# Performance work log

Measured on AMD Instinct MI355X. Metric: run time of the kernel, lower is better.

The kernel has to match this reference:

```python
import jax, jax.numpy as jnp
import numpy as np

NPOINT, RADIUS, NSAMPLE = 1024, 0.2, 32


def _fps(xyz, npoint):
    # xyz: (B, N, 3) -> (B, npoint) int32, iterative furthest point sampling
    B, N, _ = xyz.shape

    def step(carry, _):
        dists, far = carry  # (B,N), (B,)
        centroid = jnp.take_along_axis(xyz, far[:, None, None], axis=1)  # (B,1,3)
        d = jnp.sum((xyz - centroid) ** 2, axis=-1)  # (B,N)
        dists = jnp.minimum(dists, d)
        nxt = jnp.argmax(dists, axis=-1).astype(jnp.int32)
        return (dists, nxt), far

    init = (jnp.full((B, N), 1e10, xyz.dtype), jnp.zeros((B,), jnp.int32))
    _, idx = jax.lax.scan(step, init, None, length=npoint)
    return jnp.transpose(idx)  # (B, npoint)


def _ball_query(radius, nsample, xyz, new_xyz):
    # xyz: (B,N,3), new_xyz: (B,S,3) -> (B,S,nsample) int32
    N = xyz.shape[1]
    d2 = jnp.sum((new_xyz[:, :, None, :] - xyz[:, None, :, :]) ** 2, axis=-1)  # (B,S,N)
    # first-nsample-in-range semantics of PointNet++ ball_query
    key = jnp.where(d2 < radius * radius, jnp.arange(N, dtype=jnp.int32), N)
    neg, order = jax.lax.top_k(-key, nsample)  # smallest keys first
    valid = (-neg) < N
    return jnp.where(valid, order, order[..., :1])  # pad with first valid idx


def _group(feat, idx):
    # feat: (B,D,N), idx: (B,S,ns) -> (B,D,S,ns)
    return jax.vmap(lambda f, i: f[:, i])(feat, idx)


def _conv(x, w, b):
    # 1x1 Conv2d: x (B,C,S,ns), w (O,C), b (O)
    return jnp.einsum('oc,bcps->bops', w, x) + b[None, :, None, None]


def _bn(x, s, t):
    # inference BatchNorm folded into per-channel affine
    return x * s[None, :, None, None] + t[None, :, None, None]


def setup_inputs() -> dict:
    key = jax.random.key(0)
    ks = jax.random.split(key, 40)
    B, N, D = 16, 8192, 64
    BCH = 8  # max(8, 64 // 8)

    def w(k, shape, scale=0.1):
        return jax.random.normal(k, shape, jnp.float32) * scale

    def bn(k, c):
        k1, k2 = jax.random.split(k)
        return (jax.random.uniform(k1, (c,), jnp.float32, 0.75, 1.25),
                0.1 * jax.random.normal(k2, (c,), jnp.float32))

    attn_s0, attn_t0 = bn(ks[2], BCH)
    attn_s1, attn_t1 = bn(ks[3], D)
    attn_s2, attn_t2 = bn(ks[4], D)
    mlp_s0, mlp_t0 = bn(ks[5], 64)
    mlp_s1, mlp_t1 = bn(ks[6], 64)
    eca_s, eca_t = bn(ks[7], 128)
    return {
        'xyz': jax.random.uniform(ks[0], (B, 3, N), jnp.float32),
        'points': jax.random.normal(ks[1], (B, D, N), jnp.float32),
        'attn_w0': w(ks[10], (BCH, 3)), 'attn_b0': w(ks[11], (BCH,)),
        'attn_s0': attn_s0, 'attn_t0': attn_t0,
        'attn_w1': w(ks[12], (D, BCH)), 'attn_b1': w(ks[13], (D,)),
        'attn_s1': attn_s1, 'attn_t1': attn_t1,
        'attn_w2': w(ks[14], (D, D)), 'attn_b2': w(ks[15], (D,)),
        'attn_s2': attn_s2, 'attn_t2': attn_t2,
        'mlp_w0': w(ks[16], (64, D)), 'mlp_b0': w(ks[17], (64,)),
        'mlp_s0': mlp_s0, 'mlp_t0': mlp_t0,
        'mlp_w1': w(ks[18], (64, 64)), 'mlp_b1': w(ks[19], (64,)),
        'mlp_s1': mlp_s1, 'mlp_t1': mlp_t1,
        'eca_k': w(ks[20], (3,), 0.5),
        'eca_w': w(ks[21], (128, 64)), 'eca_b': w(ks[22], (128,)),
        'eca_s': eca_s, 'eca_t': eca_t,
    }


def reference(xyz, points,
              attn_w0, attn_b0, attn_s0, attn_t0,
              attn_w1, attn_b1, attn_s1, attn_t1,
              attn_w2, attn_b2, attn_s2, attn_t2,
              mlp_w0, mlp_b0, mlp_s0, mlp_t0,
              mlp_w1, mlp_b1, mlp_s1, mlp_t1,
              eca_k, eca_w, eca_b, eca_s, eca_t):
    xyz_f = jnp.transpose(xyz, (0, 2, 1))  # (B,N,3)
    # 1. sampling + grouping
    fps_idx = _fps(xyz_f, NPOINT)  # (B,S)
    new_xyz = jax.vmap(lambda p, i: p[:, i])(xyz, fps_idx)  # (B,3,S)
    idx = _ball_query(RADIUS, NSAMPLE, xyz_f, jnp.transpose(new_xyz, (0, 2, 1)))
    grouped_xyz = _group(xyz, idx) - new_xyz[..., None]  # (B,3,S,ns)
    x = _group(points, idx)  # (B,D,S,ns)
    # 2. position-attention module
    pos = jax.nn.relu(_bn(_conv(grouped_xyz, attn_w0, attn_b0), attn_s0, attn_t0))
    pos = _bn(_conv(pos, attn_w1, attn_b1), attn_s1, attn_t1)
    x = x + pos
    x = _bn(_conv(x, attn_w2, attn_b2), attn_s2, attn_t2)
    # 3. shared MLP (conv-bn-relu over mlp[:-1])
    x = jax.nn.relu(_bn(_conv(x, mlp_w0, mlp_b0), mlp_s0, mlp_t0))
    x = jax.nn.relu(_bn(_conv(x, mlp_w1, mlp_b1), mlp_s1, mlp_t1))
    # 4. ECA channel attention + final 1x1 conv-bn
    y = jnp.mean(x, axis=(2, 3))  # (B,C)
    yp = jnp.pad(y, ((0, 0), (1, 1)))
    y = eca_k[0] * yp[:, :-2] + eca_k[1] * yp[:, 1:-1] + eca_k[2] * yp[:, 2:]
    x = x * jax.nn.sigmoid(y)[:, :, None, None]
    x = _bn(_conv(x, eca_w, eca_b), eca_s, eca_t)
    # 5. max-pool over neighborhood
    new_features = jnp.max(x, axis=-1)  # (B,128,S)
    return (new_xyz, new_features)
```

## Files before the change

### kernel.cpp

```cpp
#include <hip/hip_runtime.h>

typedef unsigned int   u32;
typedef unsigned long long u64;
typedef float pkf2 __attribute__((ext_vector_type(2)));

#define B_  16
#define N_  8192
#define S_  1024
#define NS_ 32
#define XS_ 68

__device__ __forceinline__ float nanguard(float v) {
  u32 x = __float_as_uint(v);
  if ((x & 0x7F80u) == 0x7F80u) x ^= 0x0080u;
  return __uint_as_float(x);
}

__device__ __forceinline__ float wave_max_nonneg(float v) {
  int x = __float_as_int(v);
#define DPP_STEP(ctrl) \
  x = __float_as_int(fmaxf(__int_as_float(x), \
      __int_as_float(__builtin_amdgcn_update_dpp(0, x, (ctrl), 0xf, 0xf, true))))
  DPP_STEP(0x111);
  DPP_STEP(0x112);
  DPP_STEP(0x114);
  DPP_STEP(0x118);
  DPP_STEP(0x142);
  DPP_STEP(0x143);
#undef DPP_STEP
  return __int_as_float(__builtin_amdgcn_readlane(x, 63));
}

__global__ __launch_bounds__(256) void k_xyzt(const float* __restrict__ xyz, float4* __restrict__ xyzt) {
  int b = blockIdx.y;
  int i = blockIdx.x * 256 + threadIdx.x;
  const float* p = xyz + (size_t)b * 3 * N_;
  xyzt[(size_t)b * N_ + i] = make_float4(p[i], p[N_ + i], p[2 * N_ + i], 0.f);
}

__global__ __launch_bounds__(256) void k_ptst(const float* __restrict__ pts, float* __restrict__ ptst) {
  __shared__ float tile[64][65];
  int b = blockIdx.y, n0 = blockIdx.x * 64, t = threadIdx.x;
  {
    int c = t >> 2, j0 = (t & 3) * 16;
    const float4* src = (const float4*)(pts + (size_t)b * 64 * N_ + (size_t)c * N_ + n0 + j0);
#pragma unroll
    for (int q = 0; q < 4; ++q) {
      float4 a = src[q];
      tile[c][j0 + 4*q + 0] = a.x; tile[c][j0 + 4*q + 1] = a.y;
      tile[c][j0 + 4*q + 2] = a.z; tile[c][j0 + 4*q + 3] = a.w;
    }
  }
  __syncthreads();
  {
    int n = t >> 2, c0 = (t & 3) * 16;
    float4* dv = (float4*)(ptst + ((size_t)b * N_ + n0 + n) * 64 + c0);
#pragma unroll
    for (int q = 0; q < 4; ++q)
      dv[q] = make_float4(tile[c0 + 4*q + 0][n], tile[c0 + 4*q + 1][n],
                          tile[c0 + 4*q + 2][n], tile[c0 + 4*q + 3][n]);
  }
}

__global__ __launch_bounds__(1024)
__attribute__((amdgpu_waves_per_eu(4, 4)))
void k_fps(const float4* __restrict__ xyzt,
           float4* __restrict__ nxf,
           float* __restrict__ out_xyz) {
#pragma clang fp contract(off)
  __shared__ float4 ldsp[N_];
  __shared__ u64 slot[4];
  __shared__ int win_hist[S_];
  int b = blockIdx.x, t = threadIdx.x;
  const float4* p4 = xyzt + (size_t)b * N_;
  const float4* pp8 = p4 + t * 8;

  float4 q0 = pp8[0], q1 = pp8[1], q2 = pp8[2], q3 = pp8[3];
  float4 q4 = pp8[4], q5 = pp8[5], q6 = pp8[6], q7 = pp8[7];
  ldsp[t * 8 + 0] = q0; ldsp[t * 8 + 1] = q1; ldsp[t * 8 + 2] = q2; ldsp[t * 8 + 3] = q3;
  ldsp[t * 8 + 4] = q4; ldsp[t * 8 + 5] = q5; ldsp[t * 8 + 6] = q6; ldsp[t * 8 + 7] = q7;

#define DECLPAIR(P, A, B) \
  pkf2 px##P = {q##A.x, q##B.x}; pkf2 py##P = {q##A.y, q##B.y}; \
  pkf2 pz##P = {q##A.z, q##B.z}; pkf2 dm##P = {1e10f, 1e10f};
  DECLPAIR(01, 0, 1) DECLPAIR(23, 2, 3) DECLPAIR(45, 4, 5) DECLPAIR(67, 6, 7)
#undef DECLPAIR
#define PIN(P) asm volatile("" : "+v"(px##P), "+v"(py##P), "+v"(pz##P));
  PIN(01) PIN(23) PIN(45) PIN(67)
#undef PIN

  if (t == 0) {
    slot[0] = 8191ull;
    slot[1] = 0; slot[2] = 0; slot[3] = 0;
    win_hist[0] = 0;
  }
  __syncthreads();
  int lane = t & 63;
  for (int it = 1; it < S_; ++it) {
    u64 w = slot[(it - 1) & 3];
    int widx = 8191 - (int)(w & 0xFFFFFFFFull);
    if (t == 0) { win_hist[it - 1] = widx; slot[(it + 1) & 3] = 0; }
    float4 c = ldsp[widx & (N_ - 1)];
    pkf2 cx2 = {c.x, c.x}, cy2 = {c.y, c.y}, cz2 = {c.z, c.z};
#define UPDP(P) { \
    pkf2 dx = px##P - cx2; pkf2 dy = py##P - cy2; pkf2 dz = pz##P - cz2; \
    pkf2 xx = dx * dx; pkf2 yy = dy * dy; pkf2 zz = dz * dz; \
    pkf2 ss = xx + yy; pkf2 dd = ss + zz; \
    dm##P.x = fminf(dm##P.x, dd.x); dm##P.y = fminf(dm##P.y, dd.y); }
    UPDP(01) UPDP(23) UPDP(45) UPDP(67)
#undef UPDP
    float e0 = dm01.x, e1 = dm01.y, e2 = dm23.x, e3 = dm23.y;
    float e4 = dm45.x, e5 = dm45.y, e6 = dm67.x, e7 = dm67.y;
    float va0 = e1 > e0 ? e1 : e0; int ia0 = e1 > e0 ? 1 : 0;
    float va1 = e3 > e2 ? e3 : e2; int ia1 = e3 > e2 ? 3 : 2;
    float va2 = e5 > e4 ? e5 : e4; int ia2 = e5 > e4 ? 5 : 4;
    float va3 = e7 > e6 ? e7 : e6; int ia3 = e7 > e6 ? 7 : 6;
    float vb0 = va1 > va0 ? va1 : va0; int ib0 = va1 > va0 ? ia1 : ia0;
    float vb1 = va3 > va2 ? va3 : va2; int ib1 = va3 > va2 ? ia3 : ia2;
    float bv = vb1 > vb0 ? vb1 : vb0;  int bk = vb1 > vb0 ? ib1 : ib0;
    int bi = t * 8 + bk;
    float wm = wave_max_nonneg(bv);
    u64 msk = __ballot(bv == wm);
    int wl = __ffsll((long long)msk) - 1;
    int wbi = __builtin_amdgcn_readlane(bi, wl);
    if (lane == 0)
      atomicMax(&slot[it & 3],
                ((u64)__float_as_uint(wm) << 32) | (u64)(u32)(8191 - wbi));
    __syncthreads();
  }
  if (t == 0)
    win_hist[S_ - 1] = 8191 - (int)(slot[(S_ - 1) & 3] & 0xFFFFFFFFull);
  __syncthreads();
  {
    int wi = win_hist[t] & (N_ - 1);
    float4 c = ldsp[wi];
    nxf[(size_t)b * S_ + t] = c;
    float* o = out_xyz + (size_t)b * 3 * S_;
    o[t] = nanguard(c.x); o[S_ + t] = nanguard(c.y); o[2 * S_ + t] = nanguard(c.z);
  }
}

__global__ __launch_bounds__(256) void k_ball(const float4* __restrict__ xyzt,
                                              const float4* __restrict__ nxf,
                                              int* __restrict__ ballidx) {
  int gw = blockIdx.x * 4 + (threadIdx.x >> 6);
  int lane = threadIdx.x & 63;
  int b = gw >> 10, s = gw & 1023;
  float4 c = nxf[(size_t)b * S_ + s];
  const float4* pts = xyzt + (size_t)b * N_;
  int* out = ballidx + (size_t)gw * NS_;
  int cnt = 0, first = 0;
  bool havefirst = false;
  for (int chunk = 0; chunk < N_; chunk += 64) {
    float4 p = pts[chunk + lane];
    float dx = p.x - c.x, dy = p.y - c.y, dz = p.z - c.z;
    float d2 = __fadd_rn(__fadd_rn(__fmul_rn(dx, dx), __fmul_rn(dy, dy)), __fmul_rn(dz, dz));
    bool v = d2 <= 0.04f;
    u64 m = __ballot(v);
    if (m) {
      int pos = cnt + __popcll(m & ((1ull << lane) - 1ull));
      if (v && pos < NS_) out[pos] = chunk + lane;
      if (!havefirst) { first = chunk + (__ffsll((long long)m) - 1); havefirst = true; }
      cnt += __popcll(m);
      if (cnt >= NS_) break;
    }
  }
  if (cnt < NS_) {
    for (int p = cnt + lane; p < NS_; p += 64) out[p] = first;
  }
}

struct ChainSm {
  float Wbuf[64 * XS_];
  float W1f[64 * 9];
  float W0f[8 * 4];
  float s2f[64], sm0f[64], sm1f[64];
  float bb0[8];
  float bb1[64], bb2[64], bm0[64], bm1[64];
  float X[32 * XS_];
  float H[32 * XS_];
  float scratch[384];
  int   idx_s[NS_];
};

__device__ __forceinline__ void stage_w64(float* Wbuf, const float* w, int t) {
  int c = t >> 2, q = (t & 3) * 16;
  const float4* src = (const float4*)(w + c * 64 + q);
  float4* dst = (float4*)(Wbuf + c * XS_ + q);
  dst[0] = src[0]; dst[1] = src[1]; dst[2] = src[2]; dst[3] = src[3];
}

template<bool RELU>
__device__ __forceinline__ void gemm64(const float* __restrict__ Wbuf,
                                       const float* __restrict__ Xin,
                                       float* __restrict__ Yout,
                                       const float* __restrict__ scl,
                                       const float* __restrict__ bia,
                                       int lane, int n0) {
  float acc[8] = {0,0,0,0,0,0,0,0};
#pragma unroll
  for (int k4 = 0; k4 < 16; ++k4) {
    float4 wq = *(const float4*)&Wbuf[lane * XS_ + k4 * 4];
#pragma unroll
    for (int nj = 0; nj < 8; ++nj) {
      float4 xq = *(const float4*)&Xin[(n0 + nj) * XS_ + k4 * 4];
      acc[nj] += wq.x * xq.x; acc[nj] += wq.y * xq.y;
      acc[nj] += wq.z * xq.z; acc[nj] += wq.w * xq.w;
    }
  }
  float sc = scl[lane], bi = bia[lane];
#pragma unroll
  for (int nj = 0; nj < 8; ++nj) {
    float v = sc * acc[nj] + bi;
    Yout[(n0 + nj) * XS_ + lane] = RELU ? fmaxf(v, 0.f) : v;
  }
}

template<bool USE_PTST>
__device__ __forceinline__ void chain_tile(ChainSm& sm, int b, int s, int bs,
    const float4* xyzt, const float* ptst, const float* points,
    const float4* nxf, const int* ballidx,
    const float* w0, const float* b0, const float* s0, const float* t0,
    const float* w1, const float* b1, const float* s1, const float* t1,
    const float* w2, const float* b2, const float* s2, const float* t2,
    const float* m0w, const float* m0b, const float* m0s, const float* m0t,
    const float* m1w, const float* m1b, const float* m1s, const float* m1t) {
  int t = threadIdx.x, lane = t & 63, g = t >> 6, n0 = g * 8;

  stage_w64(sm.Wbuf, w2, t);
  if (t < 64) {
    float v2 = s2[t];  sm.s2f[t] = v2;  sm.bb2[t] = v2 * b2[t] + t2[t];
    float vm0 = m0s[t]; sm.sm0f[t] = vm0; sm.bm0[t] = vm0 * m0b[t] + m0t[t];
    float vm1 = m1s[t]; sm.sm1f[t] = vm1; sm.bm1[t] = vm1 * m1b[t] + m1t[t];
    float v1 = s1[t];
#pragma unroll
    for (int k = 0; k < 8; ++k) sm.W1f[t * 9 + k] = v1 * w1[t * 8 + k];
    sm.bb1[t] = v1 * b1[t] + t1[t];
  }
  if (t < 8) {
    float v0 = s0[t];
#pragma unroll
    for (int k = 0; k < 3; ++k) sm.W0f[t * 4 + k] = v0 * w0[t * 3 + k];
    sm.bb0[t] = v0 * b0[t] + t0[t];
  }
  if (t < NS_) sm.idx_s[t] = ballidx[(size_t)bs * NS_ + t] & (N_ - 1);
  __syncthreads();

  {
    int n = t >> 3, c8 = (t & 7) * 8;
    int pi = sm.idx_s[n];
    if (USE_PTST) {
      const float4* v = (const float4*)(ptst + ((size_t)b * N_ + pi) * 64 + c8);
      float4* xr = (float4*)&sm.X[n * XS_ + c8];
      xr[0] = v[0]; xr[1] = v[1];
    } else {
      const float* pp = points + (size_t)b * 64 * N_ + (size_t)c8 * N_ + pi;
#pragma unroll
      for (int j = 0; j < 8; ++j) sm.X[n * XS_ + c8 + j] = pp[(size_t)j * N_];
    }
  }
  if (t < NS_) {
    float4 p = xyzt[(size_t)b * N_ + sm.idx_s[t]];
    float4 cc = nxf[(size_t)b * S_ + s];
    float* gx = &sm.scratch[256 + t * 4];
    gx[0] = p.x - cc.x; gx[1] = p.y - cc.y; gx[2] = p.z - cc.z;
  }
  __syncthreads();

  {
    int n = t >> 3, cc = t & 7;
    const float* gx = &sm.scratch[256 + n * 4];
    float a = sm.bb0[cc];
    a += sm.W0f[cc * 4 + 0] * gx[0];
    a += sm.W0f[cc * 4 + 1] * gx[1];
    a += sm.W0f[cc * 4 + 2] * gx[2];
    sm.scratch[n * 8 + cc] = fmaxf(a, 0.f);
  }
  {
#pragma unroll
    for (int nj = 0; nj < 8; ++nj) {
      float a = sm.bb1[lane];
      const float* p8 = &sm.scratch[(n0 + nj) * 8];
#pragma unroll
      for (int k = 0; k < 8; ++k) a += sm.W1f[lane * 9 + k] * p8[k];
      sm.X[(n0 + nj) * XS_ + lane] += a;
    }
  }
  gemm64<false>(sm.Wbuf, sm.X, sm.H, sm.s2f, sm.bb2, lane, n0);
  __syncthreads();
  stage_w64(sm.Wbuf, m0w, t);
  __syncthreads();
  gemm64<true>(sm.Wbuf, sm.H, sm.X, sm.sm0f, sm.bm0, lane, n0);
  __syncthreads();
  stage_w64(sm.Wbuf, m1w, t);
  __syncthreads();
  gemm64<true>(sm.Wbuf, sm.X, sm.H, sm.sm1f, sm.bm1, lane, n0);
}

template<bool USE_PTST, bool WRITE_H2>
__global__ __launch_bounds__(256) void k_chain(
    const float4* __restrict__ xyzt, const float* __restrict__ ptst,
    const float* __restrict__ points,
    const float4* __restrict__ nxf, const int* __restrict__ ballidx,
    const float* w0, const float* b0, const float* s0, const float* t0,
    const float* w1, const float* b1, const float* s1, const float* t1,
    const float* w2, const float* b2, const float* s2, const float* t2,
    const float* m0w, const float* m0b, const float* m0s, const float* m0t,
    const float* m1w, const float* m1b, const float* m1s, const float* m1t,
    float* __restrict__ h2out, float* __restrict__ partials) {
  __shared__ ChainSm sm;
  int t = threadIdx.x, bs = blockIdx.x;
  int b = bs >> 10, s = bs & 1023;
  int lane = t & 63, g = t >> 6, n0 = g * 8;

  chain_tile<USE_PTST>(sm, b, s, bs, xyzt, ptst, points, nxf, ballidx,
                       w0, b0, s0, t0, w1, b1, s1, t1, w2, b2, s2, t2,
                       m0w, m0b, m0s, m0t, m1w, m1b, m1s, m1t);

  float* psum = sm.scratch;
  float lsum = 0.f;
#pragma unroll
  for (int nj = 0; nj < 8; ++nj) {
    float r = sm.H[(n0 + nj) * XS_ + lane];
    lsum += r;
    if (WRITE_H2)
      h2out[((size_t)bs * 32 + n0 + nj) * 64 + lane] = r;
  }
  psum[lane * 5 + g] = lsum;
  __syncthreads();
  if (t < 64) {
    float v = (psum[t * 5 + 0] + psum[t * 5 + 1]) + (psum[t * 5 + 2] + psum[t * 5 + 3]);
    partials[(size_t)bs * 64 + t] = v;
  }
}

__global__ __launch_bounds__(256) void k_eca(const float* __restrict__ partials,
                                             const float* __restrict__ ecak,
                                             float* __restrict__ sig) {
  __shared__ float red[64 * 5];
  __shared__ float yy[66];
  int b = blockIdx.x, t = threadIdx.x;
  int c = t & 63, sg = t >> 6;
  float acc = 0.f;
  for (int s = sg; s < S_; s += 4) acc += partials[((size_t)b * S_ + s) * 64 + c];
  red[c * 5 + sg] = acc;
  __syncthreads();
  if (t < 64) {
    float v = (red[t * 5 + 0] + red[t * 5 + 1]) + (red[t * 5 + 2] + red[t * 5 + 3]);
    yy[t + 1] = v * (1.f / 32768.f);
  }
  if (t == 64) { yy[0] = 0.f; yy[65] = 0.f; }
  __syncthreads();
  if (t < 64) {
    float gv = ecak[0] * yy[t] + ecak[1] * yy[t + 1] + ecak[2] * yy[t + 2];
    sig[b * 64 + t] = 1.f / (1.f + expf(-gv));
  }
}

__device__ __forceinline__ void final_gemm(const float* __restrict__ WA,
                                           const float* __restrict__ WB,
                                           const float* __restrict__ X2,
                                           const float* __restrict__ esf,
                                           const float* __restrict__ bbf,
                                           float* __restrict__ zred,
                                           float* __restrict__ outf,
                                           int b, int s, int t) {
  int lane = t & 63, g = t >> 6, n0 = g * 8;
  float aA[8] = {0,0,0,0,0,0,0,0}, aB[8] = {0,0,0,0,0,0,0,0};
#pragma unroll
  for (int k4 = 0; k4 < 16; ++k4) {
    float4 wqA = *(const float4*)&WA[lane * XS_ + k4 * 4];
    float4 wqB = *(const float4*)&WB[lane * XS_ + k4 * 4];
#pragma unroll
    for (int nj = 0; nj < 8; ++nj) {
      float4 xq = *(const float4*)&X2[(n0 + nj) * XS_ + k4 * 4];
      aA[nj] += wqA.x * xq.x; aA[nj] += wqA.y * xq.y;
      aA[nj] += wqA.z * xq.z; aA[nj] += wqA.w * xq.w;
      aB[nj] += wqB.x * xq.x; aB[nj] += wqB.y * xq.y;
      aB[nj] += wqB.z * xq.z; aB[nj] += wqB.w * xq.w;
    }
  }
  float mA = aA[0], mB = aB[0];
#pragma unroll
  for (int j = 1; j < 8; ++j) { mA = fmaxf(mA, aA[j]); mB = fmaxf(mB, aB[j]); }
  zred[lane * 5 + g]        = esf[lane] * mA + bbf[lane];
  zred[(lane + 64) * 5 + g] = esf[lane + 64] * mB + bbf[lane + 64];
  __syncthreads();
  if (t < 128) {
    float m = fmaxf(fmaxf(zred[t * 5 + 0], zred[t * 5 + 1]),
                    fmaxf(zred[t * 5 + 2], zred[t * 5 + 3]));
    outf[((size_t)b * 128 + t) * S_ + s] = nanguard(m);
  }
}

__global__ __launch_bounds__(256) void k_final_h2(const float* __restrict__ h2,
                                                  const float* __restrict__ sig,
                                                  const float* ew, const float* eb,
                                                  const float* es, const float* et,
                                                  float* __restrict__ outf) {
  __shared__ float Wh[128 * XS_];
  __shared__ float esf[128], bbf[128], sigl[64];
  __shared__ float X2[32 * XS_];
  __shared__ float zred[128 * 5];
  int t = threadIdx.x, bs = blockIdx.x;
  int b = bs >> 10, s = bs & 1023;
  {
    int c2 = t >> 1, h = (t & 1) * 32;
    const float4* src = (const float4*)(ew + c2 * 64 + h);
    float4* dst = (float4*)(Wh + c2 * XS_ + h);
#pragma unroll
    for (int j = 0; j < 8; ++j) dst[j] = src[j];
  }
  if (t < 128) {
    float v = es[t]; esf[t] = v; bbf[t] = v * eb[t] + et[t];
  }
  if (t < 64) sigl[t] = sig[b * 64 + t];
  __syncthreads();
  {
    int n = t >> 3, c8 = (t & 7) * 8;
    const float4* v = (const float4*)(h2 + ((size_t)bs * 32 + n) * 64 + c8);
    float4 a = v[0], bq = v[1];
    a.x *= sigl[c8 + 0]; a.y *= sigl[c8 + 1]; a.z *= sigl[c8 + 2]; a.w *= sigl[c8 + 3];
    bq.x *= sigl[c8 + 4]; bq.y *= sigl[c8 + 5]; bq.z *= sigl[c8 + 6]; bq.w *= sigl[c8 + 7];
    float4* xr = (float4*)&X2[n * XS_ + c8];
    xr[0] = a; xr[1] = bq;
  }
  final_gemm(Wh, Wh + 64 * XS_, X2, esf, bbf, zred, outf, b, s, t);
}

template<bool USE_PTST>
__global__ __launch_bounds__(256) void k_final_rec(
    const float4* __restrict__ xyzt, const float* __restrict__ ptst,
    const float* __restrict__ points,
    const float4* __restrict__ nxf, const int* __restrict__ ballidx,
    const float* w0, const float* b0, const float* s0, const float* t0,
    const float* w1, const float* b1, const float* s1, const float* t1,
    const float* w2, const float* b2, const float* s2, const float* t2,
    const float* m0w, const float* m0b, const float* m0s, const float* m0t,
    const float* m1w, const float* m1b, const float* m1s, const float* m1t,
    const float* __restrict__ sig,
    const float* ew, const float* eb, const float* es, const float* et,
    float* __restrict__ outf) {
  __shared__ ChainSm sm;
  __shared__ float Wb2[64 * XS_];
  __shared__ float esf2[128], bbf2[128], sigl2[64];
  __shared__ float zred[128 * 5];
  int t = threadIdx.x, bs = blockIdx.x;
  int b = bs >> 10, s = bs & 1023;
  int lane = t & 63, g = t >> 6, n0 = g * 8;

  chain_tile<USE_PTST>(sm, b, s, bs, xyzt, ptst, points, nxf, ballidx,
                       w0, b0, s0, t0, w1, b1, s1, t1, w2, b2, s2, t2,
                       m0w, m0b, m0s, m0t, m1w, m1b, m1s, m1t);

  __syncthreads();
  stage_w64(sm.Wbuf, ew, t);
  stage_w64(Wb2, ew + 64 * 64, t);
  if (t < 128) {
    float v = es[t]; esf2[t] = v; bbf2[t] = v * eb[t] + et[t];
  }
  if (t < 64) sigl2[t] = sig[b * 64 + t];
  __syncthreads();
  {
#pragma unroll
    for (int nj = 0; nj < 8; ++nj)
      sm.X[(n0 + nj) * XS_ + lane] = sigl2[lane] * sm.H[(n0 + nj) * XS_ + lane];
  }
  final_gemm(sm.Wbuf, Wb2, sm.X, esf2, bbf2, zred, outf, b, s, t);
}

extern "C" void kernel_launch(void* const* d_in, const int* in_sizes, int n_in,
                              void* d_out, int out_size, void* d_ws, size_t ws_size,
                              hipStream_t stream) {
  const float* xyz    = (const float*)d_in[0];
  const float* points = (const float*)d_in[1];
  const float* w0 = (const float*)d_in[2],  *b0 = (const float*)d_in[3],  *s0 = (const float*)d_in[4],  *t0 = (const float*)d_in[5];
  const float* w1 = (const float*)d_in[6],  *b1 = (const float*)d_in[7],  *s1 = (const float*)d_in[8],  *t1 = (const float*)d_in[9];
  const float* w2 = (const float*)d_in[10], *b2 = (const float*)d_in[11], *s2 = (const float*)d_in[12], *t2 = (const float*)d_in[13];
  const float* m0w = (const float*)d_in[14], *m0b = (const float*)d_in[15], *m0s = (const float*)d_in[16], *m0t = (const float*)d_in[17];
  const float* m1w = (const float*)d_in[18], *m1b = (const float*)d_in[19], *m1s = (const float*)d_in[20], *m1t = (const float*)d_in[21];
  const float* ecak = (const float*)d_in[22];
  const float* ew = (const float*)d_in[23], *eb = (const float*)d_in[24], *es = (const float*)d_in[25], *et = (const float*)d_in[26];

  const size_t OFF_XYZT = 0;
  const size_t OFF_NXF  = 2097152;
  const size_t OFF_BIDX = 2359296;
  const size_t OFF_PART = 4456448;
  const size_t OFF_SIG  = 8650752;
  const size_t OFF_PTST = 8654848;
  const size_t OFF_H2   = 42209280;
  const size_t NEED_PTST = OFF_H2;
  const size_t NEED_H2   = 176427008;

  const bool use_ptst = ws_size >= NEED_PTST;
  const bool use_h2   = ws_size >= NEED_H2;

  char* ws = (char*)d_ws;
  float4* xyzt    = (float4*)(ws + OFF_XYZT);
  float4* nxf     = (float4*)(ws + OFF_NXF);
  int*    ballidx = (int*)   (ws + OFF_BIDX);
  float*  partials= (float*) (ws + OFF_PART);
  float*  sig     = (float*) (ws + OFF_SIG);
  float*  ptst    = (float*) (ws + OFF_PTST);
  float*  h2      = (float*) (ws + OFF_H2);

  float* out_xyz  = (float*)d_out;
  float* out_feat = (float*)d_out + (size_t)B_ * 3 * S_;

  k_xyzt<<<dim3(N_ / 256, B_), 256, 0, stream>>>(xyz, xyzt);
  if (use_ptst)
    k_ptst<<<dim3(N_ / 64, B_), 256, 0, stream>>>(points, ptst);
  k_fps <<<B_, 1024, 0, stream>>>(xyzt, nxf, out_xyz);
  k_ball<<<(B_ * S_) / 4, 256, 0, stream>>>(xyzt, nxf, ballidx);

  if (use_h2) {
    k_chain<true, true><<<B_ * S_, 256, 0, stream>>>(xyzt, ptst, points, nxf, ballidx,
        w0, b0, s0, t0, w1, b1, s1, t1, w2, b2, s2, t2,
        m0w, m0b, m0s, m0t, m1w, m1b, m1s, m1t, h2, partials);
    k_eca<<<B_, 256, 0, stream>>>(partials, ecak, sig);
    k_final_h2<<<B_ * S_, 256, 0, stream>>>(h2, sig, ew, eb, es, et, out_feat);
  } else if (use_ptst) {
    k_chain<true, false><<<B_ * S_, 256, 0, stream>>>(xyzt, ptst, points, nxf, ballidx,
        w0, b0, s0, t0, w1, b1, s1, t1, w2, b2, s2, t2,
        m0w, m0b, m0s, m0t, m1w, m1b, m1s, m1t, h2, partials);
    k_eca<<<B_, 256, 0, stream>>>(partials, ecak, sig);
    k_final_rec<true><<<B_ * S_, 256, 0, stream>>>(xyzt, ptst, points, nxf, ballidx,
        w0, b0, s0, t0, w1, b1, s1, t1, w2, b2, s2, t2,
        m0w, m0b, m0s, m0t, m1w, m1b, m1s, m1t, sig, ew, eb, es, et, out_feat);
  } else {
    k_chain<false, false><<<B_ * S_, 256, 0, stream>>>(xyzt, ptst, points, nxf, ballidx,
        w0, b0, s0, t0, w1, b1, s1, t1, w2, b2, s2, t2,
        m0w, m0b, m0s, m0t, m1w, m1b, m1s, m1t, h2, partials);
    k_eca<<<B_, 256, 0, stream>>>(partials, ecak, sig);
    k_final_rec<false><<<B_ * S_, 256, 0, stream>>>(xyzt, ptst, points, nxf, ballidx,
        w0, b0, s0, t0, w1, b1, s1, t1, w2, b2, s2, t2,
        m0w, m0b, m0s, m0t, m1w, m1b, m1s, m1t, sig, ew, eb, es, et, out_feat);
  }
}
```

Measured before the change: 1.535 ms.

## Fuse FPS, ball query and MLP chain into one persistent producer-consumer kernel

Replaces the separate FPS, ball-query and chain launches with one persistent kernel. Sixteen blocks run furthest point sampling and publish their progress through global atomic counters. The remaining 240 worker blocks spin-wait on those counters, then run the ball query and the conv/MLP chain for each ready centroid. This overlaps the serial FPS with the per-centroid MLP work, which previously ran strictly after it. In exchange it relies on all blocks being co-resident (deadlock risk if they are not), adds spin-wait overhead, and runs the work blocks at 1024 threads with large LDS use.

```diff
diff --git a/kernel.cpp b/kernel.cpp
--- a/kernel.cpp
+++ b/kernel.cpp
@@ -9,6 +9,8 @@
 #define S_  1024
 #define NS_ 32
 #define XS_ 68
+#define NWORK_ 240
+#define NCHUNK_ 4096
 
 __device__ __forceinline__ float nanguard(float v) {
   u32 x = __float_as_uint(v);
@@ -31,7 +33,9 @@
   return __int_as_float(__builtin_amdgcn_readlane(x, 63));
 }
 
-__global__ __launch_bounds__(256) void k_xyzt(const float* __restrict__ xyz, float4* __restrict__ xyzt) {
+__global__ __launch_bounds__(256) void k_xyzt(const float* __restrict__ xyz, float4* __restrict__ xyzt,
+                                              u32* __restrict__ prog) {
+  if (blockIdx.x == 0 && blockIdx.y == 0 && threadIdx.x < 16) prog[threadIdx.x] = 0u;
   int b = blockIdx.y;
   int i = blockIdx.x * 256 + threadIdx.x;
   const float* p = xyz + (size_t)b * 3 * N_;
@@ -334,6 +338,250 @@
   }
 }
 
+struct ChainSub {
+  float X[32 * XS_];
+  float H[32 * XS_];
+  float scratch[384];
+  int   idx_s[NS_];
+};
+struct WkSm {
+  float Wc2[64 * XS_];
+  float Wm0[64 * XS_];
+  float Wm1[64 * XS_];
+  float W1f[64 * 9];
+  float W0f[8 * 4];
+  float s2f[64], sm0f[64], sm1f[64];
+  float bb0[8];
+  float bb1[64], bb2[64], bm0[64], bm1[64];
+  ChainSub sub[4];
+};
+struct FpsSm {
+  float4 ldsp[N_];
+  u64 slot[4];
+  int win_hist[S_];
+};
+union FusedSm { FpsSm f; WkSm w; };
+static_assert(sizeof(FusedSm) <= 160 * 1024, "LDS overflow");
+
+__global__ __launch_bounds__(1024)
+__attribute__((amdgpu_waves_per_eu(4, 4)))
+void k_fused(const float4* __restrict__ xyzt, const float* __restrict__ ptst,
+             float4* __restrict__ nxf, float* __restrict__ out_xyz,
+             u32* __restrict__ prog,
+             const float* w0, const float* b0, const float* s0, const float* t0,
+             const float* w1, const float* b1, const float* s1, const float* t1,
+             const float* w2, const float* b2, const float* s2, const float* t2,
+             const float* m0w, const float* m0b, const float* m0s, const float* m0t,
+             const float* m1w, const float* m1b, const float* m1s, const float* m1t,
+             float* __restrict__ h2out, float* __restrict__ partials) {
+  __shared__ FusedSm smu;
+  int t = threadIdx.x;
+
+  if (blockIdx.x < B_) {
+#pragma clang fp contract(off)
+    FpsSm& fs = smu.f;
+    int b = blockIdx.x;
+    const float4* p4 = xyzt + (size_t)b * N_;
+    const float4* pp8 = p4 + t * 8;
+
+    float4 q0 = pp8[0], q1 = pp8[1], q2 = pp8[2], q3 = pp8[3];
+    float4 q4 = pp8[4], q5 = pp8[5], q6 = pp8[6], q7 = pp8[7];
+    fs.ldsp[t * 8 + 0] = q0; fs.ldsp[t * 8 + 1] = q1; fs.ldsp[t * 8 + 2] = q2; fs.ldsp[t * 8 + 3] = q3;
+    fs.ldsp[t * 8 + 4] = q4; fs.ldsp[t * 8 + 5] = q5; fs.ldsp[t * 8 + 6] = q6; fs.ldsp[t * 8 + 7] = q7;
+
+#define DECLPAIR(P, A, B) \
+    pkf2 px##P = {q##A.x, q##B.x}; pkf2 py##P = {q##A.y, q##B.y}; \
+    pkf2 pz##P = {q##A.z, q##B.z}; pkf2 dm##P = {1e10f, 1e10f};
+    DECLPAIR(01, 0, 1) DECLPAIR(23, 2, 3) DECLPAIR(45, 4, 5) DECLPAIR(67, 6, 7)
+#undef DECLPAIR
+#define PIN(P) asm volatile("" : "+v"(px##P), "+v"(py##P), "+v"(pz##P));
+    PIN(01) PIN(23) PIN(45) PIN(67)
+#undef PIN
+
+    if (t == 0) {
+      fs.slot[0] = 8191ull;
+      fs.slot[1] = 0; fs.slot[2] = 0; fs.slot[3] = 0;
+      fs.win_hist[0] = 0;
+    }
+    __syncthreads();
+    int lane = t & 63;
+    for (int it = 1; it < S_; ++it) {
+      u64 w = fs.slot[(it - 1) & 3];
+      int widx = 8191 - (int)(w & 0xFFFFFFFFull);
+      float4 c = fs.ldsp[widx & (N_ - 1)];
+      if (t == 0) {
+        fs.win_hist[it - 1] = widx; fs.slot[(it + 1) & 3] = 0;
+        if ((it & 15) == 0)
+          __hip_atomic_store(&prog[b], (u32)(it - 1), __ATOMIC_RELEASE, __HIP_MEMORY_SCOPE_AGENT);
+        nxf[(size_t)b * S_ + (it - 1)] = c;
+      }
+      pkf2 cx2 = {c.x, c.x}, cy2 = {c.y, c.y}, cz2 = {c.z, c.z};
+#define UPDP(P) { \
+      pkf2 dx = px##P - cx2; pkf2 dy = py##P - cy2; pkf2 dz = pz##P - cz2; \
+      pkf2 xx = dx * dx; pkf2 yy = dy * dy; pkf2 zz = dz * dz; \
+      pkf2 ss = xx + yy; pkf2 dd = ss + zz; \
+      dm##P.x = fminf(dm##P.x, dd.x); dm##P.y = fminf(dm##P.y, dd.y); }
+      UPDP(01) UPDP(23) UPDP(45) UPDP(67)
+#undef UPDP
+      float e0 = dm01.x, e1 = dm01.y, e2 = dm23.x, e3 = dm23.y;
+      float e4 = dm45.x, e5 = dm45.y, e6 = dm67.x, e7 = dm67.y;
+      float va0 = e1 > e0 ? e1 : e0; int ia0 = e1 > e0 ? 1 : 0;
+      float va1 = e3 > e2 ? e3 : e2; int ia1 = e3 > e2 ? 3 : 2;
+      float va2 = e5 > e4 ? e5 : e4; int ia2 = e5 > e4 ? 5 : 4;
+      float va3 = e7 > e6 ? e7 : e6; int ia3 = e7 > e6 ? 7 : 6;
+      float vb0 = va1 > va0 ? va1 : va0; int ib0 = va1 > va0 ? ia1 : ia0;
+      float vb1 = va3 > va2 ? va3 : va2; int ib1 = va3 > va2 ? ia3 : ia2;
+      float bv = vb1 > vb0 ? vb1 : vb0;  int bk = vb1 > vb0 ? ib1 : ib0;
+      int bi = t * 8 + bk;
+      float wm = wave_max_nonneg(bv);
+      u64 msk = __ballot(bv == wm);
+      int wl = __ffsll((long long)msk) - 1;
+      int wbi = __builtin_amdgcn_readlane(bi, wl);
+      if (lane == 0)
+        atomicMax(&fs.slot[it & 3],
+                  ((u64)__float_as_uint(wm) << 32) | (u64)(u32)(8191 - wbi));
+      __syncthreads();
+    }
+    if (t == 0) {
+      int wl_ = 8191 - (int)(fs.slot[(S_ - 1) & 3] & 0xFFFFFFFFull);
+      fs.win_hist[S_ - 1] = wl_;
+      float4 c = fs.ldsp[wl_ & (N_ - 1)];
+      nxf[(size_t)b * S_ + (S_ - 1)] = c;
+    }
+    __syncthreads();
+    {
+      int wi = fs.win_hist[t] & (N_ - 1);
+      float4 c = fs.ldsp[wi];
+      float* o = out_xyz + (size_t)b * 3 * S_;
+      o[t] = nanguard(c.x); o[S_ + t] = nanguard(c.y); o[2 * S_ + t] = nanguard(c.z);
+    }
+    if (t == 0)
+      __hip_atomic_store(&prog[b], (u32)S_, __ATOMIC_RELEASE, __HIP_MEMORY_SCOPE_AGENT);
+    return;
+  }
+
+  WkSm& wk = smu.w;
+  int w = blockIdx.x - B_;
+  if (t < 256) {
+    stage_w64(wk.Wc2, w2, t);
+    stage_w64(wk.Wm0, m0w, t);
+    stage_w64(wk.Wm1, m1w, t);
+  }
+  if (t < 64) {
+    float v2 = s2[t];  wk.s2f[t] = v2;  wk.bb2[t] = v2 * b2[t] + t2[t];
+    float vm0 = m0s[t]; wk.sm0f[t] = vm0; wk.bm0[t] = vm0 * m0b[t] + m0t[t];
+    float vm1 = m1s[t]; wk.sm1f[t] = vm1; wk.bm1[t] = vm1 * m1b[t] + m1t[t];
+    float v1 = s1[t];
+#pragma unroll
+    for (int k = 0; k < 8; ++k) wk.W1f[t * 9 + k] = v1 * w1[t * 8 + k];
+    wk.bb1[t] = v1 * b1[t] + t1[t];
+  }
+  if (t < 8) {
+    float v0 = s0[t];
+#pragma unroll
+    for (int k = 0; k < 3; ++k) wk.W0f[t * 4 + k] = v0 * w0[t * 3 + k];
+    wk.bb0[t] = v0 * b0[t] + t0[t];
+  }
+  __syncthreads();
+
+  int sg = t >> 8, tid = t & 255, lane = t & 63, g2 = (t >> 6) & 3, n0 = g2 * 8;
+  ChainSub& cs = wk.sub[sg];
+
+  for (int c = w; c < NCHUNK_; c += NWORK_) {
+    int s = c >> 2, bg = c & 3, b = bg * 4 + sg;
+    if (t == 0) {
+      int bbase = bg * 4;
+#pragma unroll
+      for (int j = 0; j < 4; ++j) {
+        while (__hip_atomic_load(&prog[bbase + j], __ATOMIC_RELAXED, __HIP_MEMORY_SCOPE_AGENT) < (u32)(s + 1))
+          __builtin_amdgcn_s_sleep(32);
+      }
+      (void)__hip_atomic_load(&prog[bbase], __ATOMIC_ACQUIRE, __HIP_MEMORY_SCOPE_AGENT);
+    }
+    __syncthreads();
+
+    float4 cc;
+    if (g2 == 0) {
+      cc = nxf[(size_t)b * S_ + s];
+      const float4* pts = xyzt + (size_t)b * N_;
+      int cnt = 0, first = 0;
+      bool havefirst = false;
+      for (int chunk = 0; chunk < N_; chunk += 64) {
+        float4 p = pts[chunk + lane];
+        float dx = p.x - cc.x, dy = p.y - cc.y, dz = p.z - cc.z;
+        float d2 = __fadd_rn(__fadd_rn(__fmul_rn(dx, dx), __fmul_rn(dy, dy)), __fmul_rn(dz, dz));
+        bool v = d2 <= 0.04f;
+        u64 m = __ballot(v);
+        if (m) {
+          int pos = cnt + __popcll(m & ((1ull << lane) - 1ull));
+          if (v && pos < NS_) cs.idx_s[pos] = chunk + lane;
+          if (!havefirst) { first = chunk + (__ffsll((long long)m) - 1); havefirst = true; }
+          cnt += __popcll(m);
+          if (cnt >= NS_) break;
+        }
+      }
+      if (cnt < NS_) {
+        for (int p = cnt + lane; p < NS_; p += 64) cs.idx_s[p] = first;
+      }
+    }
+    __syncthreads();
+
+    {
+      int n = tid >> 3, c8 = (tid & 7) * 8;
+      int pi = cs.idx_s[n];
+      const float4* v = (const float4*)(ptst + ((size_t)b * N_ + pi) * 64 + c8);
+      float4* xr = (float4*)&cs.X[n * XS_ + c8];
+      xr[0] = v[0]; xr[1] = v[1];
+    }
+    if (tid < NS_) {
+      float4 p = xyzt[(size_t)b * N_ + cs.idx_s[tid]];
+      float* gx = &cs.scratch[256 + tid * 4];
+      gx[0] = p.x - cc.x; gx[1] = p.y - cc.y; gx[2] = p.z - cc.z;
+    }
+    __syncthreads();
+
+    {
+      int n = tid >> 3, ch = tid & 7;
+      const float* gx = &cs.scratch[256 + n * 4];
+      float a = wk.bb0[ch];
+      a += wk.W0f[ch * 4 + 0] * gx[0];
+      a += wk.W0f[ch * 4 + 1] * gx[1];
+      a += wk.W0f[ch * 4 + 2] * gx[2];
+      cs.scratch[n * 8 + ch] = fmaxf(a, 0.f);
+    }
+    {
+#pragma unroll
+      for (int nj = 0; nj < 8; ++nj) {
+        float a = wk.bb1[lane];
+        const float* p8 = &cs.scratch[(n0 + nj) * 8];
+#pragma unroll
+        for (int k = 0; k < 8; ++k) a += wk.W1f[lane * 9 + k] * p8[k];
+        cs.X[(n0 + nj) * XS_ + lane] += a;
+      }
+    }
+    gemm64<false>(wk.Wc2, cs.X, cs.H, wk.s2f, wk.bb2, lane, n0);
+    gemm64<true >(wk.Wm0, cs.H, cs.X, wk.sm0f, wk.bm0, lane, n0);
+    gemm64<true >(wk.Wm1, cs.X, cs.H, wk.sm1f, wk.bm1, lane, n0);
+
+    int bs = (b << 10) | s;
+    float lsum = 0.f;
+#pragma unroll
+    for (int nj = 0; nj < 8; ++nj) {
+      float r = cs.H[(n0 + nj) * XS_ + lane];
+      lsum += r;
+      h2out[((size_t)bs * 32 + n0 + nj) * 64 + lane] = r;
+    }
+    __syncthreads();
+    cs.scratch[lane * 5 + g2] = lsum;
+    __syncthreads();
+    if (tid < 64) {
+      float v = (cs.scratch[tid * 5 + 0] + cs.scratch[tid * 5 + 1]) +
+                (cs.scratch[tid * 5 + 2] + cs.scratch[tid * 5 + 3]);
+      partials[(size_t)bs * 64 + tid] = v;
+    }
+  }
+}
+
 __global__ __launch_bounds__(256) void k_eca(const float* __restrict__ partials,
                                              const float* __restrict__ ecak,
                                              float* __restrict__ sig) {
@@ -499,6 +747,7 @@
   float4* xyzt    = (float4*)(ws + OFF_XYZT);
   float4* nxf     = (float4*)(ws + OFF_NXF);
   int*    ballidx = (int*)   (ws + OFF_BIDX);
+  u32*    prog    = (u32*)   (ws + OFF_BIDX);
   float*  partials= (float*) (ws + OFF_PART);
   float*  sig     = (float*) (ws + OFF_SIG);
   float*  ptst    = (float*) (ws + OFF_PTST);
@@ -507,19 +756,19 @@
   float* out_xyz  = (float*)d_out;
   float* out_feat = (float*)d_out + (size_t)B_ * 3 * S_;
 
-  k_xyzt<<<dim3(N_ / 256, B_), 256, 0, stream>>>(xyz, xyzt);
+  k_xyzt<<<dim3(N_ / 256, B_), 256, 0, stream>>>(xyz, xyzt, prog);
   if (use_ptst)
     k_ptst<<<dim3(N_ / 64, B_), 256, 0, stream>>>(points, ptst);
-  k_fps <<<B_, 1024, 0, stream>>>(xyzt, nxf, out_xyz);
-  k_ball<<<(B_ * S_) / 4, 256, 0, stream>>>(xyzt, nxf, ballidx);
 
   if (use_h2) {
-    k_chain<true, true><<<B_ * S_, 256, 0, stream>>>(xyzt, ptst, points, nxf, ballidx,
+    k_fused<<<B_ + NWORK_, 1024, 0, stream>>>(xyzt, ptst, nxf, out_xyz, prog,
         w0, b0, s0, t0, w1, b1, s1, t1, w2, b2, s2, t2,
         m0w, m0b, m0s, m0t, m1w, m1b, m1s, m1t, h2, partials);
     k_eca<<<B_, 256, 0, stream>>>(partials, ecak, sig);
     k_final_h2<<<B_ * S_, 256, 0, stream>>>(h2, sig, ew, eb, es, et, out_feat);
   } else if (use_ptst) {
+    k_fps <<<B_, 1024, 0, stream>>>(xyzt, nxf, out_xyz);
+    k_ball<<<(B_ * S_) / 4, 256, 0, stream>>>(xyzt, nxf, ballidx);
     k_chain<true, false><<<B_ * S_, 256, 0, stream>>>(xyzt, ptst, points, nxf, ballidx,
         w0, b0, s0, t0, w1, b1, s1, t1, w2, b2, s2, t2,
         m0w, m0b, m0s, m0t, m1w, m1b, m1s, m1t, h2, partials);
@@ -528,6 +777,8 @@
         w0, b0, s0, t0, w1, b1, s1, t1, w2, b2, s2, t2,
         m0w, m0b, m0s, m0t, m1w, m1b, m1s, m1t, sig, ew, eb, es, et, out_feat);
   } else {
+    k_fps <<<B_, 1024, 0, stream>>>(xyzt, nxf, out_xyz);
+    k_ball<<<(B_ * S_) / 4, 256, 0, stream>>>(xyzt, nxf, ballidx);
     k_chain<false, false><<<B_ * S_, 256, 0, stream>>>(xyzt, ptst, points, nxf, ballidx,
         w0, b0, s0, t0, w1, b1, s1, t1, w2, b2, s2, t2,
         m0w, m0b, m0s, m0t, m1w, m1b, m1s, m1t, h2, partials);
```

Measured after the change: 1.240 ms. -19.2%, faster.
